# Performance work log

Hardware: AMD Instinct MI355X
Metric: run time of the kernel (lower is better)

The kernel has to match this reference:

```python
import math
import jax, jax.numpy as jnp
import numpy as np

B, S, D, E, K, H = 4, 1024, 768, 8, 2, 2048
NH_ROUTER, NH_COLLAB = 12, 2  # collab heads = min(n_heads, top_k) = 2
EPS = 1e-5


def setup_inputs() -> dict:
    key = jax.random.key(0)
    ks = jax.random.split(key, 16)
    n = lambda k, shp, s=0.02: jax.random.normal(k, shp, jnp.float32) * s
    return {
        "x": jax.random.normal(ks[0], (B, S, D), jnp.float32),
        # parallel expert params (E, D, H) / (E, H, D)
        "w1": n(ks[1], (E, D, H)), "w3": n(ks[2], (E, D, H)), "w2": n(ks[3], (E, H, D)),
        # router self-attention (torch MultiheadAttention packed qkv + out proj)
        "r_in_w": n(ks[4], (3 * D, D)), "r_in_b": jnp.zeros((3 * D,), jnp.float32),
        "r_out_w": n(ks[5], (D, D)), "r_out_b": jnp.zeros((D,), jnp.float32),
        "r_norm_w": jnp.ones((D,), jnp.float32),
        "gate_w": n(ks[6], (E, D)),
        # collaborative cross-attention
        "c_in_w": n(ks[7], (3 * D, D)), "c_in_b": jnp.zeros((3 * D,), jnp.float32),
        "c_out_w": n(ks[8], (D, D)), "c_out_b": jnp.zeros((D,), jnp.float32),
        "c_norm_w": jnp.ones((D,), jnp.float32),
        "ffn_w1": n(ks[9], (D, D)), "ffn_w2": n(ks[10], (D, D)),
        "o_w": n(ks[11], (D, D)),
    }


def _mha(x, in_w, in_b, out_w, out_b, nh):
    # torch nn.MultiheadAttention, batch_first, q=k=v=x; returns out and head-avg probs
    N, L, Dm = x.shape
    hd = Dm // nh
    qkv = x @ in_w.T + in_b                       # (N, L, 3D)
    q, k, v = jnp.split(qkv, 3, axis=-1)
    sp = lambda t: t.reshape(N, L, nh, hd).transpose(0, 2, 1, 3)
    q, k, v = sp(q), sp(k), sp(v)
    probs = jax.nn.softmax(jnp.einsum('nhld,nhmd->nhlm', q, k) / math.sqrt(hd), axis=-1)
    o = jnp.einsum('nhlm,nhmd->nhld', probs, v).transpose(0, 2, 1, 3).reshape(N, L, Dm)
    return o @ out_w.T + out_b, probs.mean(axis=1)


def _rms(x, w):
    return x * jax.lax.rsqrt(jnp.mean(x * x, axis=-1, keepdims=True) + EPS) * w


def reference(x, w1, w3, w2, r_in_w, r_in_b, r_out_w, r_out_b, r_norm_w, gate_w,
              c_in_w, c_in_b, c_out_w, c_out_b, c_norm_w, ffn_w1, ffn_w2, o_w):
    Bx, Sx, Dx = x.shape
    # dense all-expert SwiGLU: (B,S,E,D)
    gate = jnp.einsum('bsd,edh->bseh', x, w1)
    up = jnp.einsum('bsd,edh->bseh', x, w3)
    expert_out = jnp.einsum('bseh,ehd->bsed', jax.nn.silu(gate) * up, w2)
    ef = expert_out.reshape(Bx * Sx, E, Dx)
    # attention-based router over the E experts per token
    ctx, _ = _mha(ef, r_in_w, r_in_b, r_out_w, r_out_b, NH_ROUTER)
    ctx = _rms(ctx + ef, r_norm_w)
    logits = (ctx.mean(axis=1) @ gate_w.T).reshape(Bx, Sx, E)
    routing_probs = jax.nn.softmax(logits, axis=-1)
    tk_logits, tk_idx = jax.lax.top_k(logits, K)  # router_temperature = 1.0
    tk_probs = jax.nn.softmax(tk_logits, axis=-1)
    sel = jnp.take_along_axis(expert_out, tk_idx[..., None], axis=2)  # (B,S,K,D)
    sf = sel.reshape(Bx * Sx, K, Dx)
    # collaborative fusion among selected experts
    ao, aw = _mha(sf, c_in_w, c_in_b, c_out_w, c_out_b, NH_COLLAB)
    ao = _rms(ao + sf, c_norm_w)
    refined = (jax.nn.gelu(ao @ ffn_w1.T, approximate=False) @ ffn_w2.T) + ao
    refined = refined.reshape(Bx, Sx, K, Dx)
    final = jnp.sum(refined * tk_probs[..., None], axis=2) @ o_w.T
    # auxiliary loss
    usage = routing_probs.mean(axis=(0, 1))
    balance = jnp.mean((usage - usage.mean()) ** 2)
    diversity = jnp.mean(-jnp.sum(aw * jnp.log(aw + 1e-9), axis=-1))
    aux = 0.1 * (0.01 * diversity + 0.01 * balance)
    return final, aux, tk_idx
```

## Files before the change

### kernel.cpp

```cpp
#include <hip/hip_runtime.h>


typedef unsigned short u16;
typedef unsigned int u32;
typedef _Float16 f16;
typedef f16 f16x4 __attribute__((ext_vector_type(4)));
typedef f16 f16x8 __attribute__((ext_vector_type(8)));
typedef float f32x4 __attribute__((ext_vector_type(4)));

__device__ __forceinline__ float b2f(u16 v){
  union { u32 u; float f; } x; x.u = ((u32)v) << 16; return x.f;
}
__device__ __forceinline__ u16 f2b(float f){
  union { float f; u32 u; } x; x.f = f;
  u32 u = x.u;
  if ((u & 0x7fffffffu) > 0x7f800000u) return (u16)0x7fc0;
  return (u16)((u + 0x7fffu + ((u >> 16) & 1u)) >> 16);
}
__device__ __forceinline__ float gelu_f(float x){
  return 0.5f * x * (1.f + erff(x * 0.70710678118654752f));
}

template<int NW>
__device__ __forceinline__ float blockReduceSum(float v, float* red){
  #pragma unroll
  for (int o = 32; o > 0; o >>= 1) v += __shfl_down(v, o, 64);
  const int wv = threadIdx.x >> 6, ln = threadIdx.x & 63;
  __syncthreads();
  if (ln == 0) red[wv] = v;
  __syncthreads();
  float s = 0.f;
  #pragma unroll
  for (int i = 0; i < NW; i++) s += red[i];
  return s;
}

__device__ __forceinline__ float waveReduceSum(float v){
  #pragma unroll
  for (int o = 32; o > 0; o >>= 1) v += __shfl_xor(v, o, 64);
  return v;
}

template<int AK, bool SPLIT, bool BT, bool BIAS, int ACT, bool RES, bool DUAL, bool SK2>
__global__ __launch_bounds__(256, 2) void mgemm(
    const void* __restrict__ Ap, int lda, long long strideA,
    const float* __restrict__ B1, const float* __restrict__ B2, int ldb, long long strideB,
    float* __restrict__ C1, float* __restrict__ C2, int ldc, long long strideC,
    const float* __restrict__ bias, const float* __restrict__ resid, int ldr,
    int Kd, int zs)
{
  __shared__ f16 AsH[2][128*40];
  __shared__ f16 BsH[2][128*40];
  __shared__ f16 AsL[SPLIT ? 2 : 1][SPLIT ? 128*40 : 4];
  __shared__ f16 BsL[SPLIT ? 2 : 1][SPLIT ? 128*40 : 4];

  const int tid = threadIdx.x;
  const int m0 = blockIdx.y * 128, n0 = blockIdx.x * 128;
  const int z = blockIdx.z;
  int zi = z, k0 = 0, KL = Kd;
  const float* Bz; float* Cz;
  if constexpr (DUAL){
    if (z < zs){ zi = z;      Bz = B1 + (long long)zi*strideB; Cz = C1 + (long long)zi*strideC; }
    else       { zi = z - zs; Bz = B2 + (long long)zi*strideB; Cz = C2 + (long long)zi*strideC; }
  } else if constexpr (SK2){
    const int s = (z >= zs) ? 1 : 0;
    zi = z - s * zs;
    KL = Kd >> 1; k0 = s * KL;
    Bz = B1 + (long long)zi*strideB + (BT ? (long long)k0 : (long long)k0 * ldb);
    Cz = (s ? C2 : C1) + (long long)zi*strideC;
  } else {
    Bz = B1 + (long long)z*strideB; Cz = C1 + (long long)z*strideC;
  }
  const float* A32 = (const float*)Ap + (AK==0 ? (long long)zi*strideA : 0) + k0;
  const u16*   A16 = (const u16*)Ap   + (AK==1 ? (long long)zi*strideA : 0) + k0;

  const int ln = tid & 63, wv = tid >> 6;
  const int wm = (wv >> 1) * 64, wn = (wv & 1) * 64;
  const int fr = ln & 15, fq = ln >> 4;

  const int rA = tid >> 1, kcA = (tid & 1) * 16;
  const int npB = tid & 63, kgB = tid >> 6;

  f32x4 av[4]; uint4 av16[2]; f32x4 bv[4]; float2 bw[8];

  auto loadAB = [&](int kt){
    if constexpr (AK == 0){
      const float* s = A32 + (size_t)(m0 + rA) * lda + kt + kcA;
      av[0] = ((const f32x4*)s)[0]; av[1] = ((const f32x4*)s)[1];
      av[2] = ((const f32x4*)s)[2]; av[3] = ((const f32x4*)s)[3];
    } else {
      const u16* s = A16 + (size_t)(m0 + rA) * lda + kt + kcA;
      av16[0] = ((const uint4*)s)[0]; av16[1] = ((const uint4*)s)[1];
    }
    if constexpr (BT){
      const float* s = Bz + (size_t)(n0 + rA) * ldb + kt + kcA;
      bv[0] = ((const f32x4*)s)[0]; bv[1] = ((const f32x4*)s)[1];
      bv[2] = ((const f32x4*)s)[2]; bv[3] = ((const f32x4*)s)[3];
    } else {
      const float* s = Bz + (size_t)(kt + kgB * 8) * ldb + n0 + 2 * npB;
      #pragma unroll
      for (int kk = 0; kk < 8; kk++) bw[kk] = *(const float2*)(s + (size_t)kk * ldb);
    }
  };

  auto storeAB = [&](int b){
    if constexpr (AK == 0){
      #pragma unroll
      for (int jj = 0; jj < 2; jj++){
        f16x8 h, l;
        #pragma unroll
        for (int c = 0; c < 8; c++){
          const float v = av[jj*2 + (c>>2)][c & 3];
          h[c] = (f16)v;
          if constexpr (SPLIT) l[c] = (f16)(v - (float)h[c]);
        }
        *(f16x8*)&AsH[b][rA*40 + kcA + jj*8] = h;
        if constexpr (SPLIT) *(f16x8*)&AsL[b][rA*40 + kcA + jj*8] = l;
      }
    } else {
      #pragma unroll
      for (int j = 0; j < 2; j++){
        const uint4 v = av16[j];
        f16x8 h;
        h[0]=(f16)b2f((u16)(v.x & 0xffff)); h[1]=(f16)b2f((u16)(v.x >> 16));
        h[2]=(f16)b2f((u16)(v.y & 0xffff)); h[3]=(f16)b2f((u16)(v.y >> 16));
        h[4]=(f16)b2f((u16)(v.z & 0xffff)); h[5]=(f16)b2f((u16)(v.z >> 16));
        h[6]=(f16)b2f((u16)(v.w & 0xffff)); h[7]=(f16)b2f((u16)(v.w >> 16));
        *(f16x8*)&AsH[b][rA*40 + kcA + j*8] = h;
      }
    }
    if constexpr (BT){
      #pragma unroll
      for (int jj = 0; jj < 2; jj++){
        f16x8 h, l;
        #pragma unroll
        for (int c = 0; c < 8; c++){
          const float v = bv[jj*2 + (c>>2)][c & 3];
          h[c] = (f16)v;
          if constexpr (SPLIT) l[c] = (f16)(v - (float)h[c]);
        }
        *(f16x8*)&BsH[b][rA*40 + kcA + jj*8] = h;
        if constexpr (SPLIT) *(f16x8*)&BsL[b][rA*40 + kcA + jj*8] = l;
      }
    } else {
      #pragma unroll
      for (int c = 0; c < 2; c++){
        const int row = 2*npB + c;
        const int p8 = (kgB + (row >> 2)) & 3;
        f16x8 h, l;
        #pragma unroll
        for (int kk = 0; kk < 8; kk++){
          const float v = c ? bw[kk].y : bw[kk].x;
          h[kk] = (f16)v;
          if constexpr (SPLIT) l[kk] = (f16)(v - (float)h[kk]);
        }
        *(f16x8*)&BsH[b][row*40 + p8*8] = h;
        if constexpr (SPLIT) *(f16x8*)&BsL[b][row*40 + p8*8] = l;
      }
    }
  };

  f32x4 acc[4][4];
  #pragma unroll
  for (int i = 0; i < 4; i++)
    #pragma unroll
    for (int j = 0; j < 4; j++){ acc[i][j][0]=0.f; acc[i][j][1]=0.f; acc[i][j][2]=0.f; acc[i][j][3]=0.f; }

  int aoff[4], boff[4];
  #pragma unroll
  for (int i = 0; i < 4; i++) aoff[i] = (wm + i*16 + fr)*40 + fq*8;
  #pragma unroll
  for (int j = 0; j < 4; j++){
    const int brow = wn + j*16 + fr;
    boff[j] = brow*40 + (BT ? fq*8 : (((fq + (brow >> 2)) & 3) << 3));
  }

  loadAB(0);
  const int NT = KL >> 5;
  for (int t = 0; t < NT; t++){
    const int b = t & 1;
    storeAB(b);
    __syncthreads();
    if (t + 1 < NT) loadAB((t + 1) << 5);
    f16x8 aH[4], bH[4];
    #pragma unroll
    for (int i = 0; i < 4; i++) aH[i] = *(const f16x8*)&AsH[b][aoff[i]];
    #pragma unroll
    for (int j = 0; j < 4; j++) bH[j] = *(const f16x8*)&BsH[b][boff[j]];
    #pragma unroll
    for (int i = 0; i < 4; i++)
      #pragma unroll
      for (int j = 0; j < 4; j++)
        acc[i][j] = __builtin_amdgcn_mfma_f32_16x16x32_f16(aH[i], bH[j], acc[i][j], 0, 0, 0);
    if constexpr (SPLIT){
      f16x8 aL[4], bL[4];
      #pragma unroll
      for (int i = 0; i < 4; i++) aL[i] = *(const f16x8*)&AsL[b][aoff[i]];
      #pragma unroll
      for (int j = 0; j < 4; j++) bL[j] = *(const f16x8*)&BsL[b][boff[j]];
      #pragma unroll
      for (int i = 0; i < 4; i++)
        #pragma unroll
        for (int j = 0; j < 4; j++){
          acc[i][j] = __builtin_amdgcn_mfma_f32_16x16x32_f16(aH[i], bL[j], acc[i][j], 0, 0, 0);
          acc[i][j] = __builtin_amdgcn_mfma_f32_16x16x32_f16(aL[i], bH[j], acc[i][j], 0, 0, 0);
        }
    }
  }

  #pragma unroll
  for (int j = 0; j < 4; j++){
    const int n = n0 + wn + j*16 + fr;
    float bvv = 0.f;
    if constexpr (BIAS) bvv = bias[n];
    #pragma unroll
    for (int i = 0; i < 4; i++){
      #pragma unroll
      for (int r = 0; r < 4; r++){
        const int m = m0 + wm + i*16 + fq*4 + r;
        float v = acc[i][j][r];
        if constexpr (BIAS) v += bvv;
        if constexpr (ACT == 1) v = gelu_f(v);
        if constexpr (RES) v += resid[(size_t)m * ldr + n];
        Cz[(size_t)m * ldc + n] = v;
      }
    }
  }
}

__global__ void silu_k(const float4* __restrict__ g, const float4* __restrict__ u,
                       float4* __restrict__ h, int n4){
  const int i = blockIdx.x * 256 + threadIdx.x;
  if (i < n4){
    const float4 gv = g[i], uv = u[i];
    float4 r;
    r.x = (gv.x / (1.f + expf(-gv.x))) * uv.x;
    r.y = (gv.y / (1.f + expf(-gv.y))) * uv.y;
    r.z = (gv.z / (1.f + expf(-gv.z))) * uv.z;
    r.w = (gv.w / (1.f + expf(-gv.w))) * uv.w;
    h[i] = r;
  }
}

template<int ACT, bool RES, bool BIAS>
__global__ void add2_k(float* __restrict__ dst, const float* __restrict__ src,
                       const float* __restrict__ bias, const float* __restrict__ resid,
                       int n4, int ld4){
  const int i = blockIdx.x * 256 + threadIdx.x;
  if (i >= n4) return;
  const f32x4 a = ((const f32x4*)dst)[i];
  const f32x4 b = ((const f32x4*)src)[i];
  const int c4 = (i % ld4) * 4;
  f32x4 r;
  #pragma unroll
  for (int c = 0; c < 4; c++){
    float v = a[c] + b[c];
    if constexpr (BIAS) v += bias[c4 + c];
    if constexpr (ACT == 1) v = gelu_f(v);
    if constexpr (RES) v += resid[(size_t)i * 4 + c];
    r[c] = v;
  }
  ((f32x4*)dst)[i] = r;
}

__global__ __launch_bounds__(128) void router_attn(const float* __restrict__ qkv,
                                                   float* __restrict__ attn_o){
  __shared__ float L[8 * 1536];
  __shared__ float Ps[96][8];
  const int t = blockIdx.x, tid = threadIdx.x;
  const float* src = qkv + (size_t)t * 8 * 2304;
  for (int i = tid; i < 3072; i += 128){
    const int e = i / 384, c4 = i - e * 384;
    ((float4*)L)[i] = ((const float4*)(src + (size_t)e * 2304))[c4];
  }
  __syncthreads();
  if (tid < 96){
    const int h = tid >> 3, e = tid & 7;
    const float* q = L + e * 1536 + h * 64;
    float s[8]; float mx = -1e30f;
    #pragma unroll
    for (int e2 = 0; e2 < 8; e2++){
      const float* kk = L + e2 * 1536 + 768 + h * 64;
      float acc = 0.f;
      #pragma unroll
      for (int d = 0; d < 64; d++) acc = fmaf(q[d], kk[d], acc);
      s[e2] = acc * 0.125f;
      mx = fmaxf(mx, s[e2]);
    }
    float den = 0.f;
    #pragma unroll
    for (int e2 = 0; e2 < 8; e2++){ s[e2] = expf(s[e2] - mx); den += s[e2]; }
    const float inv = 1.f / den;
    #pragma unroll
    for (int e2 = 0; e2 < 8; e2++) Ps[tid][e2] = s[e2] * inv;
  }
  __syncthreads();
  for (int i = tid; i < 1536; i += 128){
    const int e = i / 192, c4 = i - e * 192;
    ((float4*)L)[i] = ((const float4*)(src + (size_t)e * 2304 + 1536))[c4];
  }
  __syncthreads();
  if (tid < 96){
    const int h = tid >> 3, e = tid & 7;
    float p[8];
    #pragma unroll
    for (int e2 = 0; e2 < 8; e2++) p[e2] = Ps[tid][e2];
    float* dst = attn_o + ((size_t)t * 8 + e) * 768 + h * 64;
    for (int d = 0; d < 64; d++){
      float acc = 0.f;
      #pragma unroll
      for (int e2 = 0; e2 < 8; e2++) acc = fmaf(p[e2], L[e2 * 768 + h * 64 + d], acc);
      dst[d] = acc;
    }
  }
}

__global__ __launch_bounds__(256) void router_final(
    const float* __restrict__ proj, const float* __restrict__ eoc,
    const float* __restrict__ rnw, const float* __restrict__ gw,
    int t0, float* __restrict__ usage, float* __restrict__ tkp,
    u16* __restrict__ sf, float* __restrict__ oidx)
{
  const int wv = threadIdx.x >> 6, ln = threadIdx.x & 63;
  const int tl = blockIdx.x * 4 + wv, t = t0 + tl;

  float rw[12];
  #pragma unroll
  for (int g = 0; g < 3; g++){
    const f32x4 w = ((const f32x4*)rnw)[ln + g * 64];
    #pragma unroll
    for (int c = 0; c < 4; c++) rw[g*4 + c] = w[c];
  }

  float cs[12];
  #pragma unroll
  for (int i = 0; i < 12; i++) cs[i] = 0.f;

  for (int e = 0; e < 8; e++){
    const float* pr = proj + ((size_t)tl * 8 + e) * 768;
    const float* er = eoc  + ((size_t)tl * 8 + e) * 768;
    float v[12]; float ss = 0.f;
    #pragma unroll
    for (int g = 0; g < 3; g++){
      const f32x4 a = ((const f32x4*)pr)[ln + g * 64];
      const f32x4 b = ((const f32x4*)er)[ln + g * 64];
      #pragma unroll
      for (int c = 0; c < 4; c++){ const float vv = a[c] + b[c]; v[g*4 + c] = vv; ss += vv * vv; }
    }
    ss = waveReduceSum(ss);
    const float sc = 1.f / sqrtf(ss * (1.f / 768.f) + 1e-5f);
    #pragma unroll
    for (int i = 0; i < 12; i++) cs[i] += v[i] * sc * rw[i];
  }

  float lg[8];
  #pragma unroll
  for (int j = 0; j < 8; j++){
    const float* gwr = gw + j * 768;
    float p = 0.f;
    #pragma unroll
    for (int g = 0; g < 3; g++){
      const f32x4 w = ((const f32x4*)gwr)[ln + g * 64];
      #pragma unroll
      for (int c = 0; c < 4; c++) p += cs[g*4 + c] * w[c];
    }
    lg[j] = waveReduceSum(p) * 0.125f;
  }

  int i0 = 0; float l0 = lg[0];
  #pragma unroll
  for (int j = 1; j < 8; j++) if (lg[j] > l0){ l0 = lg[j]; i0 = j; }
  int i1 = -1; float l1 = -1e30f;
  #pragma unroll
  for (int j = 0; j < 8; j++) if (j != i0 && lg[j] > l1){ l1 = lg[j]; i1 = j; }

  if (ln == 0){
    float mx = -1e30f;
    #pragma unroll
    for (int j = 0; j < 8; j++) mx = fmaxf(mx, lg[j]);
    float ex[8], den = 0.f;
    #pragma unroll
    for (int j = 0; j < 8; j++){ ex[j] = expf(lg[j] - mx); den += ex[j]; }
    const float inv = 1.f / den;
    #pragma unroll
    for (int j = 0; j < 8; j++) atomicAdd(&usage[j], ex[j] * inv);
    const float e1 = expf(l1 - l0);
    const float p0 = 1.f / (1.f + e1);
    tkp[(size_t)t * 2]     = p0;
    tkp[(size_t)t * 2 + 1] = e1 * p0;
    oidx[(size_t)t * 2]     = (float)i0;
    oidx[(size_t)t * 2 + 1] = (float)i1;
  }

  #pragma unroll
  for (int s = 0; s < 2; s++){
    const int ie = s ? i1 : i0;
    const float* er = eoc + ((size_t)tl * 8 + ie) * 768;
    #pragma unroll
    for (int g = 0; g < 3; g++){
      const f32x4 a = ((const f32x4*)er)[ln + g * 64];
      ushort4 o;
      o.x = f2b(a[0]); o.y = f2b(a[1]); o.z = f2b(a[2]); o.w = f2b(a[3]);
      *(ushort4*)&sf[((size_t)t * 2 + s) * 768 + 4 * (ln + g * 64)] = o;
    }
  }
}

__global__ __launch_bounds__(128) void collab_attn(
    const float* __restrict__ qkv, float* __restrict__ attn_o, float* __restrict__ divsum)
{
  const int t = blockIdx.x, tid = threadIdx.x;
  __shared__ float L[4608];
  __shared__ float P[8];
  __shared__ float red[2];
  const float* src = qkv + (size_t)t * 4608;
  for (int i = tid; i < 4608; i += 128) L[i] = src[i];
  __syncthreads();
  for (int hij = 0; hij < 8; hij++){
    const int h = hij >> 2, qi = (hij >> 1) & 1, kj = hij & 1;
    const float* q = L + qi * 2304 + h * 384;
    const float* k = L + kj * 2304 + 768 + h * 384;
    float acc = 0.f;
    for (int d = tid; d < 384; d += 128) acc += q[d] * k[d];
    acc = blockReduceSum<2>(acc, red);
    if (tid == 0) P[hij] = acc;
  }
  __syncthreads();
  if (tid == 0){
    const float scale = 0.051031036307982884f;
    float aw[2][2] = {{0.f,0.f},{0.f,0.f}};
    for (int h = 0; h < 2; h++)
      for (int i = 0; i < 2; i++){
        const float s0 = P[h*4 + i*2 + 0] * scale, s1 = P[h*4 + i*2 + 1] * scale;
        const float m = fmaxf(s0, s1);
        const float e0 = expf(s0 - m), e1 = expf(s1 - m), inv = 1.f / (e0 + e1);
        P[h*4 + i*2 + 0] = e0 * inv; P[h*4 + i*2 + 1] = e1 * inv;
        aw[i][0] += 0.5f * e0 * inv; aw[i][1] += 0.5f * e1 * inv;
      }
    float ent = 0.f;
    for (int i = 0; i < 2; i++)
      for (int j = 0; j < 2; j++) ent -= aw[i][j] * logf(aw[i][j] + 1e-9f);
    atomicAdd(divsum, ent);
  }
  __syncthreads();
  for (int c = tid; c < 768; c += 128){
    const int h = c / 384;
    const float v0 = L[1536 + c], v1 = L[3840 + c];
    attn_o[((size_t)t * 2 + 0) * 768 + c] = P[h*4 + 0] * v0 + P[h*4 + 1] * v1;
    attn_o[((size_t)t * 2 + 1) * 768 + c] = P[h*4 + 2] * v0 + P[h*4 + 3] * v1;
  }
}

__global__ __launch_bounds__(256) void rms_k(const float* __restrict__ a, const u16* __restrict__ b,
                                             const float* __restrict__ wt, float* __restrict__ o){
  const int r = blockIdx.x, tid = threadIdx.x;
  __shared__ float red[4];
  float v[3]; float ss = 0.f;
  #pragma unroll
  for (int i = 0; i < 3; i++){
    const int c = tid + i * 256;
    v[i] = a[(size_t)r * 768 + c] + b2f(b[(size_t)r * 768 + c]);
    ss += v[i] * v[i];
  }
  ss = blockReduceSum<4>(ss, red);
  const float sc = 1.f / sqrtf(ss * (1.f / 768.f) + 1e-5f);
  #pragma unroll
  for (int i = 0; i < 3; i++){
    const int c = tid + i * 256;
    o[(size_t)r * 768 + c] = v[i] * sc * wt[c];
  }
}

__global__ void wsum(const float* __restrict__ refined, const float* __restrict__ tkp,
                     float* __restrict__ y){
  const int idx = blockIdx.x * 256 + threadIdx.x;
  const int t = idx / 768, c = idx - t * 768;
  const float r0 = refined[((size_t)t * 2) * 768 + c];
  const float r1 = refined[((size_t)t * 2 + 1) * 768 + c];
  y[idx] = tkp[t * 2] * r0 + tkp[t * 2 + 1] * r1;
}

__global__ void aux_k(const float* __restrict__ usage, const float* __restrict__ divsum,
                      float* __restrict__ out){
  if (threadIdx.x == 0 && blockIdx.x == 0){
    float u[8], s = 0.f;
    for (int e = 0; e < 8; e++){ u[e] = usage[e] * (1.f / 4096.f); s += u[e]; }
    const float mean = s * 0.125f;
    float bal = 0.f;
    for (int e = 0; e < 8; e++){ const float d = u[e] - mean; bal += d * d; }
    bal *= 0.125f;
    const float div = divsum[0] * (1.f / 8192.f);
    out[0] = 0.1f * (0.01f * div + 0.01f * bal);
  }
}

__global__ void zero_k(float* p, int n){
  const int i = blockIdx.x * 64 + threadIdx.x;
  if (i < n) p[i] = 0.f;
}

extern "C" void kernel_launch(void* const* d_in, const int* in_sizes, int n_in,
                              void* d_out, int out_size, void* d_ws, size_t ws_size,
                              hipStream_t stream)
{
  (void)in_sizes; (void)n_in; (void)out_size; (void)ws_size;
  const float* x       = (const float*)d_in[0];
  const float* w1      = (const float*)d_in[1];
  const float* w3      = (const float*)d_in[2];
  const float* w2      = (const float*)d_in[3];
  const float* r_in_w  = (const float*)d_in[4];
  const float* r_in_b  = (const float*)d_in[5];
  const float* r_out_w = (const float*)d_in[6];
  const float* r_out_b = (const float*)d_in[7];
  const float* r_norm_w= (const float*)d_in[8];
  const float* gate_w  = (const float*)d_in[9];
  const float* c_in_w  = (const float*)d_in[10];
  const float* c_in_b  = (const float*)d_in[11];
  const float* c_out_w = (const float*)d_in[12];
  const float* c_out_b = (const float*)d_in[13];
  const float* c_norm_w= (const float*)d_in[14];
  const float* ffn_w1  = (const float*)d_in[15];
  const float* ffn_w2  = (const float*)d_in[16];
  const float* o_w     = (const float*)d_in[17];

  char* wsb   = (char*)d_ws;
  char* arena = wsb;
  float* eoc  = (float*)(wsb + 33554432);
  u16*   sf   = (u16*)  (wsb + 39845888);
  float* tkp  = (float*)(wsb + 52428800);
  float* usage= (float*)(wsb + 52461568);

  float* gateb = (float*)(arena);
  float* upb   = (float*)(arena + 16777216);
  float* qkvr  = (float*)(arena);
  float* aor   = (float*)(arena + 18874368);
  float* projr = (float*)(arena + 25165824);

  float* qkvc  = (float*)(arena);
  float* aoc   = (float*)(arena + 18874368);
  float* projc = (float*)(arena + 25165824);
  float* aob   = (float*)(arena);
  float* t1b   = (float*)(arena + 6291456);
  float* refb  = (float*)(arena + 12582912);
  float* ybuf  = (float*)(arena + 18874368);

  float* outp    = (float*)d_out;
  float* out_aux = outp + (size_t)4096*768;
  float* out_idx = out_aux + 1;

  zero_k<<<1, 64, 0, stream>>>(usage, 16);

  for (int cch = 0; cch < 16; cch++){
    const int t0 = cch * 256;
    mgemm<0,true,false,false,0,false,true,false><<<dim3(16,2,16),256,0,stream>>>(
      x + (size_t)t0*768, 768, 0LL,
      w1, w3, 2048, 1572864LL,
      gateb, upb, 2048, 524288LL,
      nullptr, nullptr, 0, 768, 8);
    silu_k<<<4096, 256, 0, stream>>>((const float4*)gateb, (const float4*)upb,
                                     (float4*)gateb, 1048576);
    mgemm<0,true,false,false,0,false,false,true><<<dim3(6,2,16),256,0,stream>>>(
      gateb, 2048, 524288LL,
      w2, nullptr, 768, 1572864LL,
      eoc, upb, 6144, 768LL,
      nullptr, nullptr, 0, 2048, 8);
    add2_k<0,false,false><<<1536, 256, 0, stream>>>(eoc, upb, nullptr, nullptr, 393216, 192);
    mgemm<0,true,true,true,0,false,false,false><<<dim3(18,16,1),256,0,stream>>>(
      eoc, 768, 0LL, r_in_w, nullptr, 768, 0LL,
      qkvr, nullptr, 2304, 0LL, r_in_b, nullptr, 0, 768, 0);
    router_attn<<<256, 128, 0, stream>>>(qkvr, aor);
    mgemm<0,true,true,false,0,false,false,true><<<dim3(6,16,2),256,0,stream>>>(
      aor, 768, 0LL, r_out_w, nullptr, 768, 0LL,
      projr, qkvr, 768, 0LL, nullptr, nullptr, 0, 768, 1);
    add2_k<0,false,true><<<1536, 256, 0, stream>>>(projr, qkvr, r_out_b, nullptr, 393216, 192);
    router_final<<<64, 256, 0, stream>>>(projr, eoc, r_norm_w, gate_w, t0,
                                         usage, tkp, sf, out_idx);
  }

  for (int q = 0; q < 4; q++){
    const int tq0 = q * 1024;
    const u16* sf_q = sf + (size_t)tq0 * 2 * 768;
    mgemm<1,false,true,true,0,false,false,false><<<dim3(18,16,1),256,0,stream>>>(
      sf_q, 768, 0LL, c_in_w, nullptr, 768, 0LL,
      qkvc, nullptr, 2304, 0LL, c_in_b, nullptr, 0, 768, 0);
    collab_attn<<<1024, 128, 0, stream>>>(qkvc, aoc, usage + 8);
    mgemm<0,false,true,false,0,false,false,true><<<dim3(6,16,2),256,0,stream>>>(
      aoc, 768, 0LL, c_out_w, nullptr, 768, 0LL,
      projc, qkvc, 768, 0LL, nullptr, nullptr, 0, 768, 1);
    add2_k<0,false,true><<<1536, 256, 0, stream>>>(projc, qkvc, c_out_b, nullptr, 393216, 192);
    rms_k<<<2048, 256, 0, stream>>>(projc, sf_q, c_norm_w, aob);
    mgemm<0,false,true,false,0,false,false,true><<<dim3(6,16,2),256,0,stream>>>(
      aob, 768, 0LL, ffn_w1, nullptr, 768, 0LL,
      t1b, refb, 768, 0LL, nullptr, nullptr, 0, 768, 1);
    add2_k<1,false,false><<<1536, 256, 0, stream>>>(t1b, refb, nullptr, nullptr, 393216, 192);
    mgemm<0,false,true,false,0,false,false,true><<<dim3(6,16,2),256,0,stream>>>(
      t1b, 768, 0LL, ffn_w2, nullptr, 768, 0LL,
      refb, projc, 768, 0LL, nullptr, nullptr, 0, 768, 1);
    add2_k<0,true,false><<<1536, 256, 0, stream>>>(refb, projc, nullptr, aob, 393216, 192);
    wsum<<<3072, 256, 0, stream>>>(refb, tkp + (size_t)tq0 * 2, ybuf);
    mgemm<0,false,true,false,0,false,false,true><<<dim3(6,8,2),256,0,stream>>>(
      ybuf, 768, 0LL, o_w, nullptr, 768, 0LL,
      outp + (size_t)tq0 * 768, t1b, 768, 0LL, nullptr, nullptr, 0, 768, 1);
    add2_k<0,false,false><<<768, 256, 0, stream>>>(outp + (size_t)tq0 * 768, t1b, nullptr, nullptr, 196608, 192);
  }
  aux_k<<<1, 64, 0, stream>>>(usage, usage + 8, out_aux);
}
```

Measured before the change: 4.209 ms.

## Fuse split-K reductions and elementwise ops into GEMM A-loads and consumers

Adds an A-operand prologue to the GEMM that combines two fp32 inputs while loading (SiLU*up, add of split-K partials, add+GELU). This removes the standalone silu and add2 passes, and downstream kernels (router_final, rms2, wsum3) now consume both split-K partials plus the bias directly. The main loop is restructured into a two-register-set double-buffered pipeline, and the LDS swizzle for the non-transposed B operand is changed. The cost is extra registers and redundant reads of the partial buffers in the consumers, and the output buffer is reused as scratch for the w2 partial.

```diff
diff --git a/kernel.cpp b/kernel.cpp
--- a/kernel.cpp
+++ b/kernel.cpp
@@ -41,9 +41,9 @@
   return v;
 }
 
-template<int AK, bool SPLIT, bool BT, bool BIAS, int ACT, bool RES, bool DUAL, bool SK2>
+template<int AK, int AOP, bool SPLIT, bool BT, bool BIAS, int ACT, bool RES, bool DUAL, bool SK2>
 __global__ __launch_bounds__(256, 2) void mgemm(
-    const void* __restrict__ Ap, int lda, long long strideA,
+    const void* __restrict__ Ap, const float* __restrict__ A2p, int lda, long long strideA,
     const float* __restrict__ B1, const float* __restrict__ B2, int ldb, long long strideB,
     float* __restrict__ C1, float* __restrict__ C2, int ldc, long long strideC,
     const float* __restrict__ bias, const float* __restrict__ resid, int ldr,
@@ -71,8 +71,9 @@
   } else {
     Bz = B1 + (long long)z*strideB; Cz = C1 + (long long)z*strideC;
   }
-  const float* A32 = (const float*)Ap + (AK==0 ? (long long)zi*strideA : 0) + k0;
-  const u16*   A16 = (const u16*)Ap   + (AK==1 ? (long long)zi*strideA : 0) + k0;
+  const float* A32  = (const float*)Ap + (AK==0 ? (long long)zi*strideA : 0) + k0;
+  const u16*   A16  = (const u16*)Ap   + (AK==1 ? (long long)zi*strideA : 0) + k0;
+  const float* A32b = (AOP != 0) ? (A2p + (long long)zi*strideA + k0) : nullptr;
 
   const int ln = tid & 63, wv = tid >> 6;
   const int wm = (wv >> 1) * 64, wn = (wv & 1) * 64;
@@ -81,36 +82,52 @@
   const int rA = tid >> 1, kcA = (tid & 1) * 16;
   const int npB = tid & 63, kgB = tid >> 6;
 
-  f32x4 av[4]; uint4 av16[2]; f32x4 bv[4]; float2 bw[8];
-
-  auto loadAB = [&](int kt){
+  struct Regs {
+    f32x4 av[4]; f32x4 av2[4]; uint4 av16[2]; f32x4 bv[4]; float2 bw[8];
+  };
+  Regs R0, R1;
+
+  auto loadAB = [&](Regs& R, int kt){
     if constexpr (AK == 0){
       const float* s = A32 + (size_t)(m0 + rA) * lda + kt + kcA;
-      av[0] = ((const f32x4*)s)[0]; av[1] = ((const f32x4*)s)[1];
-      av[2] = ((const f32x4*)s)[2]; av[3] = ((const f32x4*)s)[3];
+      #pragma unroll
+      for (int j = 0; j < 4; j++) R.av[j] = ((const f32x4*)s)[j];
+      if constexpr (AOP != 0){
+        const float* s2 = A32b + (size_t)(m0 + rA) * lda + kt + kcA;
+        #pragma unroll
+        for (int j = 0; j < 4; j++) R.av2[j] = ((const f32x4*)s2)[j];
+      }
     } else {
       const u16* s = A16 + (size_t)(m0 + rA) * lda + kt + kcA;
-      av16[0] = ((const uint4*)s)[0]; av16[1] = ((const uint4*)s)[1];
+      R.av16[0] = ((const uint4*)s)[0]; R.av16[1] = ((const uint4*)s)[1];
     }
     if constexpr (BT){
       const float* s = Bz + (size_t)(n0 + rA) * ldb + kt + kcA;
-      bv[0] = ((const f32x4*)s)[0]; bv[1] = ((const f32x4*)s)[1];
-      bv[2] = ((const f32x4*)s)[2]; bv[3] = ((const f32x4*)s)[3];
+      #pragma unroll
+      for (int j = 0; j < 4; j++) R.bv[j] = ((const f32x4*)s)[j];
     } else {
       const float* s = Bz + (size_t)(kt + kgB * 8) * ldb + n0 + 2 * npB;
       #pragma unroll
-      for (int kk = 0; kk < 8; kk++) bw[kk] = *(const float2*)(s + (size_t)kk * ldb);
+      for (int kk = 0; kk < 8; kk++) R.bw[kk] = *(const float2*)(s + (size_t)kk * ldb);
     }
   };
 
-  auto storeAB = [&](int b){
+  auto storeAB = [&](const Regs& R, int b){
     if constexpr (AK == 0){
       #pragma unroll
       for (int jj = 0; jj < 2; jj++){
         f16x8 h, l;
         #pragma unroll
         for (int c = 0; c < 8; c++){
-          const float v = av[jj*2 + (c>>2)][c & 3];
+          float v = R.av[jj*2 + (c>>2)][c & 3];
+          if constexpr (AOP == 1){
+            const float u = R.av2[jj*2 + (c>>2)][c & 3];
+            v = (v / (1.f + expf(-v))) * u;
+          } else if constexpr (AOP == 2){
+            v = v + R.av2[jj*2 + (c>>2)][c & 3];
+          } else if constexpr (AOP == 3){
+            v = gelu_f(v + R.av2[jj*2 + (c>>2)][c & 3]);
+          }
           h[c] = (f16)v;
           if constexpr (SPLIT) l[c] = (f16)(v - (float)h[c]);
         }
@@ -120,7 +137,7 @@
     } else {
       #pragma unroll
       for (int j = 0; j < 2; j++){
-        const uint4 v = av16[j];
+        const uint4 v = R.av16[j];
         f16x8 h;
         h[0]=(f16)b2f((u16)(v.x & 0xffff)); h[1]=(f16)b2f((u16)(v.x >> 16));
         h[2]=(f16)b2f((u16)(v.y & 0xffff)); h[3]=(f16)b2f((u16)(v.y >> 16));
@@ -135,7 +152,7 @@
         f16x8 h, l;
         #pragma unroll
         for (int c = 0; c < 8; c++){
-          const float v = bv[jj*2 + (c>>2)][c & 3];
+          const float v = R.bv[jj*2 + (c>>2)][c & 3];
           h[c] = (f16)v;
           if constexpr (SPLIT) l[c] = (f16)(v - (float)h[c]);
         }
@@ -146,11 +163,11 @@
       #pragma unroll
       for (int c = 0; c < 2; c++){
         const int row = 2*npB + c;
-        const int p8 = (kgB + (row >> 2)) & 3;
+        const int p8 = (kgB + (row >> 3)) & 3;
         f16x8 h, l;
         #pragma unroll
         for (int kk = 0; kk < 8; kk++){
-          const float v = c ? bw[kk].y : bw[kk].x;
+          const float v = c ? R.bw[kk].y : R.bw[kk].x;
           h[kk] = (f16)v;
           if constexpr (SPLIT) l[kk] = (f16)(v - (float)h[kk]);
         }
@@ -172,16 +189,10 @@
   #pragma unroll
   for (int j = 0; j < 4; j++){
     const int brow = wn + j*16 + fr;
-    boff[j] = brow*40 + (BT ? fq*8 : (((fq + (brow >> 2)) & 3) << 3));
-  }
-
-  loadAB(0);
-  const int NT = KL >> 5;
-  for (int t = 0; t < NT; t++){
-    const int b = t & 1;
-    storeAB(b);
-    __syncthreads();
-    if (t + 1 < NT) loadAB((t + 1) << 5);
+    boff[j] = brow*40 + (BT ? fq*8 : (((fq + (brow >> 3)) & 3) << 3));
+  }
+
+  auto compute = [&](int b){
     f16x8 aH[4], bH[4];
     #pragma unroll
     for (int i = 0; i < 4; i++) aH[i] = *(const f16x8*)&AsH[b][aoff[i]];
@@ -206,6 +217,20 @@
           acc[i][j] = __builtin_amdgcn_mfma_f32_16x16x32_f16(aL[i], bH[j], acc[i][j], 0, 0, 0);
         }
     }
+  };
+
+  const int NT = KL >> 5;
+  loadAB(R0, 0);
+  loadAB(R1, 32);
+  for (int tt = 0; tt < NT; tt += 2){
+    storeAB(R0, 0);
+    __syncthreads();
+    if (tt + 2 < NT) loadAB(R0, (tt + 2) << 5);
+    compute(0);
+    storeAB(R1, 1);
+    __syncthreads();
+    if (tt + 3 < NT) loadAB(R1, (tt + 3) << 5);
+    compute(1);
   }
 
   #pragma unroll
@@ -225,20 +250,6 @@
         Cz[(size_t)m * ldc + n] = v;
       }
     }
-  }
-}
-
-__global__ void silu_k(const float4* __restrict__ g, const float4* __restrict__ u,
-                       float4* __restrict__ h, int n4){
-  const int i = blockIdx.x * 256 + threadIdx.x;
-  if (i < n4){
-    const float4 gv = g[i], uv = u[i];
-    float4 r;
-    r.x = (gv.x / (1.f + expf(-gv.x))) * uv.x;
-    r.y = (gv.y / (1.f + expf(-gv.y))) * uv.y;
-    r.z = (gv.z / (1.f + expf(-gv.z))) * uv.z;
-    r.w = (gv.w / (1.f + expf(-gv.w))) * uv.w;
-    h[i] = r;
   }
 }
 
@@ -265,7 +276,7 @@
 
 __global__ __launch_bounds__(128) void router_attn(const float* __restrict__ qkv,
                                                    float* __restrict__ attn_o){
-  __shared__ float L[8 * 1536];
+  __shared__ __align__(16) float L[8 * 1536];
   __shared__ float Ps[96][8];
   const int t = blockIdx.x, tid = threadIdx.x;
   const float* src = qkv + (size_t)t * 8 * 2304;
@@ -316,7 +327,9 @@
 }
 
 __global__ __launch_bounds__(256) void router_final(
-    const float* __restrict__ proj, const float* __restrict__ eoc,
+    const float* __restrict__ proj0, const float* __restrict__ proj1,
+    const float* __restrict__ pbias,
+    const float* __restrict__ eoc0, const float* __restrict__ eoc1,
     const float* __restrict__ rnw, const float* __restrict__ gw,
     int t0, float* __restrict__ usage, float* __restrict__ tkp,
     u16* __restrict__ sf, float* __restrict__ oidx)
@@ -324,12 +337,13 @@
   const int wv = threadIdx.x >> 6, ln = threadIdx.x & 63;
   const int tl = blockIdx.x * 4 + wv, t = t0 + tl;
 
-  float rw[12];
+  float rw[12], pb[12];
   #pragma unroll
   for (int g = 0; g < 3; g++){
     const f32x4 w = ((const f32x4*)rnw)[ln + g * 64];
-    #pragma unroll
-    for (int c = 0; c < 4; c++) rw[g*4 + c] = w[c];
+    const f32x4 bbv = ((const f32x4*)pbias)[ln + g * 64];
+    #pragma unroll
+    for (int c = 0; c < 4; c++){ rw[g*4 + c] = w[c]; pb[g*4 + c] = bbv[c]; }
   }
 
   float cs[12];
@@ -337,15 +351,19 @@
   for (int i = 0; i < 12; i++) cs[i] = 0.f;
 
   for (int e = 0; e < 8; e++){
-    const float* pr = proj + ((size_t)tl * 8 + e) * 768;
-    const float* er = eoc  + ((size_t)tl * 8 + e) * 768;
+    const size_t ro = ((size_t)tl * 8 + e) * 768;
     float v[12]; float ss = 0.f;
     #pragma unroll
     for (int g = 0; g < 3; g++){
-      const f32x4 a = ((const f32x4*)pr)[ln + g * 64];
-      const f32x4 b = ((const f32x4*)er)[ln + g * 64];
-      #pragma unroll
-      for (int c = 0; c < 4; c++){ const float vv = a[c] + b[c]; v[g*4 + c] = vv; ss += vv * vv; }
+      const f32x4 p0 = ((const f32x4*)(proj0 + ro))[ln + g * 64];
+      const f32x4 p1 = ((const f32x4*)(proj1 + ro))[ln + g * 64];
+      const f32x4 e0 = ((const f32x4*)(eoc0 + ro))[ln + g * 64];
+      const f32x4 e1 = ((const f32x4*)(eoc1 + ro))[ln + g * 64];
+      #pragma unroll
+      for (int c = 0; c < 4; c++){
+        const float vv = ((p0[c] + p1[c]) + pb[g*4 + c]) + (e0[c] + e1[c]);
+        v[g*4 + c] = vv; ss += vv * vv;
+      }
     }
     ss = waveReduceSum(ss);
     const float sc = 1.f / sqrtf(ss * (1.f / 768.f) + 1e-5f);
@@ -384,10 +402,10 @@
     const float inv = 1.f / den;
     #pragma unroll
     for (int j = 0; j < 8; j++) atomicAdd(&usage[j], ex[j] * inv);
-    const float e1 = expf(l1 - l0);
-    const float p0 = 1.f / (1.f + e1);
+    const float e1v = expf(l1 - l0);
+    const float p0 = 1.f / (1.f + e1v);
     tkp[(size_t)t * 2]     = p0;
-    tkp[(size_t)t * 2 + 1] = e1 * p0;
+    tkp[(size_t)t * 2 + 1] = e1v * p0;
     oidx[(size_t)t * 2]     = (float)i0;
     oidx[(size_t)t * 2 + 1] = (float)i1;
   }
@@ -395,12 +413,14 @@
   #pragma unroll
   for (int s = 0; s < 2; s++){
     const int ie = s ? i1 : i0;
-    const float* er = eoc + ((size_t)tl * 8 + ie) * 768;
+    const size_t ro = ((size_t)tl * 8 + ie) * 768;
     #pragma unroll
     for (int g = 0; g < 3; g++){
-      const f32x4 a = ((const f32x4*)er)[ln + g * 64];
+      const f32x4 a = ((const f32x4*)(eoc0 + ro))[ln + g * 64];
+      const f32x4 b = ((const f32x4*)(eoc1 + ro))[ln + g * 64];
       ushort4 o;
-      o.x = f2b(a[0]); o.y = f2b(a[1]); o.z = f2b(a[2]); o.w = f2b(a[3]);
+      o.x = f2b(a[0] + b[0]); o.y = f2b(a[1] + b[1]);
+      o.z = f2b(a[2] + b[2]); o.w = f2b(a[3] + b[3]);
       *(ushort4*)&sf[((size_t)t * 2 + s) * 768 + 4 * (ln + g * 64)] = o;
     }
   }
@@ -410,11 +430,11 @@
     const float* __restrict__ qkv, float* __restrict__ attn_o, float* __restrict__ divsum)
 {
   const int t = blockIdx.x, tid = threadIdx.x;
-  __shared__ float L[4608];
+  __shared__ __align__(16) float L[4608];
   __shared__ float P[8];
   __shared__ float red[2];
   const float* src = qkv + (size_t)t * 4608;
-  for (int i = tid; i < 4608; i += 128) L[i] = src[i];
+  for (int i = tid; i < 1152; i += 128) ((float4*)L)[i] = ((const float4*)src)[i];
   __syncthreads();
   for (int hij = 0; hij < 8; hij++){
     const int h = hij >> 2, qi = (hij >> 1) & 1, kj = hij & 1;
@@ -451,15 +471,18 @@
   }
 }
 
-__global__ __launch_bounds__(256) void rms_k(const float* __restrict__ a, const u16* __restrict__ b,
-                                             const float* __restrict__ wt, float* __restrict__ o){
+__global__ __launch_bounds__(256) void rms2_k(
+    const float* __restrict__ a0, const float* __restrict__ a1,
+    const float* __restrict__ bb, const u16* __restrict__ rb,
+    const float* __restrict__ wt, float* __restrict__ o){
   const int r = blockIdx.x, tid = threadIdx.x;
   __shared__ float red[4];
   float v[3]; float ss = 0.f;
   #pragma unroll
   for (int i = 0; i < 3; i++){
     const int c = tid + i * 256;
-    v[i] = a[(size_t)r * 768 + c] + b2f(b[(size_t)r * 768 + c]);
+    const float t = (a0[(size_t)r * 768 + c] + a1[(size_t)r * 768 + c]) + bb[c];
+    v[i] = t + b2f(rb[(size_t)r * 768 + c]);
     ss += v[i] * v[i];
   }
   ss = blockReduceSum<4>(ss, red);
@@ -471,13 +494,15 @@
   }
 }
 
-__global__ void wsum(const float* __restrict__ refined, const float* __restrict__ tkp,
-                     float* __restrict__ y){
+__global__ void wsum3(const float* __restrict__ pA, const float* __restrict__ pB,
+                      const float* __restrict__ ao, const float* __restrict__ tkp,
+                      float* __restrict__ y){
   const int idx = blockIdx.x * 256 + threadIdx.x;
   const int t = idx / 768, c = idx - t * 768;
-  const float r0 = refined[((size_t)t * 2) * 768 + c];
-  const float r1 = refined[((size_t)t * 2 + 1) * 768 + c];
-  y[idx] = tkp[t * 2] * r0 + tkp[t * 2 + 1] * r1;
+  const size_t r0 = ((size_t)t * 2) * 768 + c, r1 = r0 + 768;
+  const float v0 = (pA[r0] + pB[r0]) + ao[r0];
+  const float v1 = (pA[r1] + pB[r1]) + ao[r1];
+  y[idx] = tkp[t * 2] * v0 + tkp[t * 2 + 1] * v1;
 }
 
 __global__ void aux_k(const float* __restrict__ usage, const float* __restrict__ divsum,
@@ -535,73 +560,71 @@
   float* qkvr  = (float*)(arena);
   float* aor   = (float*)(arena + 18874368);
   float* projr = (float*)(arena + 25165824);
+  float* pr2   = (float*)(arena);
 
   float* qkvc  = (float*)(arena);
   float* aoc   = (float*)(arena + 18874368);
-  float* projc = (float*)(arena + 25165824);
-  float* aob   = (float*)(arena);
-  float* t1b   = (float*)(arena + 6291456);
-  float* refb  = (float*)(arena + 12582912);
-  float* ybuf  = (float*)(arena + 18874368);
+  float* pc1   = (float*)(arena + 25165824);
+  float* pc2   = (float*)(arena);
+  float* aob   = (float*)(arena + 6291456);
+  float* pf1   = (float*)(arena + 12582912);
+  float* pf2   = (float*)(arena + 18874368);
+  float* ybuf  = (float*)(arena + 12582912);
+  float* fo2   = (float*)(arena + 18874368);
 
   float* outp    = (float*)d_out;
   float* out_aux = outp + (size_t)4096*768;
   float* out_idx = out_aux + 1;
+  float* w2p2    = outp;
 
   zero_k<<<1, 64, 0, stream>>>(usage, 16);
 
   for (int cch = 0; cch < 16; cch++){
     const int t0 = cch * 256;
-    mgemm<0,true,false,false,0,false,true,false><<<dim3(16,2,16),256,0,stream>>>(
-      x + (size_t)t0*768, 768, 0LL,
+    mgemm<0,0,true,false,false,0,false,true,false><<<dim3(16,2,16),256,0,stream>>>(
+      x + (size_t)t0*768, nullptr, 768, 0LL,
       w1, w3, 2048, 1572864LL,
       gateb, upb, 2048, 524288LL,
       nullptr, nullptr, 0, 768, 8);
-    silu_k<<<4096, 256, 0, stream>>>((const float4*)gateb, (const float4*)upb,
-                                     (float4*)gateb, 1048576);
-    mgemm<0,true,false,false,0,false,false,true><<<dim3(6,2,16),256,0,stream>>>(
-      gateb, 2048, 524288LL,
+    mgemm<0,1,true,false,false,0,false,false,true><<<dim3(6,2,16),256,0,stream>>>(
+      gateb, upb, 2048, 524288LL,
       w2, nullptr, 768, 1572864LL,
-      eoc, upb, 6144, 768LL,
+      eoc, w2p2, 6144, 768LL,
       nullptr, nullptr, 0, 2048, 8);
-    add2_k<0,false,false><<<1536, 256, 0, stream>>>(eoc, upb, nullptr, nullptr, 393216, 192);
-    mgemm<0,true,true,true,0,false,false,false><<<dim3(18,16,1),256,0,stream>>>(
-      eoc, 768, 0LL, r_in_w, nullptr, 768, 0LL,
+    mgemm<0,2,true,true,true,0,false,false,false><<<dim3(18,16,1),256,0,stream>>>(
+      eoc, w2p2, 768, 0LL, r_in_w, nullptr, 768, 0LL,
       qkvr, nullptr, 2304, 0LL, r_in_b, nullptr, 0, 768, 0);
     router_attn<<<256, 128, 0, stream>>>(qkvr, aor);
-    mgemm<0,true,true,false,0,false,false,true><<<dim3(6,16,2),256,0,stream>>>(
-      aor, 768, 0LL, r_out_w, nullptr, 768, 0LL,
-      projr, qkvr, 768, 0LL, nullptr, nullptr, 0, 768, 1);
-    add2_k<0,false,true><<<1536, 256, 0, stream>>>(projr, qkvr, r_out_b, nullptr, 393216, 192);
-    router_final<<<64, 256, 0, stream>>>(projr, eoc, r_norm_w, gate_w, t0,
-                                         usage, tkp, sf, out_idx);
+    mgemm<0,0,true,true,false,0,false,false,true><<<dim3(6,16,2),256,0,stream>>>(
+      aor, nullptr, 768, 0LL, r_out_w, nullptr, 768, 0LL,
+      projr, pr2, 768, 0LL, nullptr, nullptr, 0, 768, 1);
+    router_final<<<64, 256, 0, stream>>>(projr, pr2, r_out_b, eoc, w2p2,
+                                         r_norm_w, gate_w, t0, usage, tkp, sf, out_idx);
   }
 
   for (int q = 0; q < 4; q++){
     const int tq0 = q * 1024;
     const u16* sf_q = sf + (size_t)tq0 * 2 * 768;
-    mgemm<1,false,true,true,0,false,false,false><<<dim3(18,16,1),256,0,stream>>>(
-      sf_q, 768, 0LL, c_in_w, nullptr, 768, 0LL,
+    mgemm<1,0,false,true,true,0,false,false,false><<<dim3(18,16,1),256,0,stream>>>(
+      sf_q, nullptr, 768, 0LL, c_in_w, nullptr, 768, 0LL,
       qkvc, nullptr, 2304, 0LL, c_in_b, nullptr, 0, 768, 0);
     collab_attn<<<1024, 128, 0, stream>>>(qkvc, aoc, usage + 8);
-    mgemm<0,false,true,false,0,false,false,true><<<dim3(6,16,2),256,0,stream>>>(
-      aoc, 768, 0LL, c_out_w, nullptr, 768, 0LL,
-      projc, qkvc, 768, 0LL, nullptr, nullptr, 0, 768, 1);
-    add2_k<0,false,true><<<1536, 256, 0, stream>>>(projc, qkvc, c_out_b, nullptr, 393216, 192);
-    rms_k<<<2048, 256, 0, stream>>>(projc, sf_q, c_norm_w, aob);
-    mgemm<0,false,true,false,0,false,false,true><<<dim3(6,16,2),256,0,stream>>>(
-      aob, 768, 0LL, ffn_w1, nullptr, 768, 0LL,
-      t1b, refb, 768, 0LL, nullptr, nullptr, 0, 768, 1);
-    add2_k<1,false,false><<<1536, 256, 0, stream>>>(t1b, refb, nullptr, nullptr, 393216, 192);
-    mgemm<0,false,true,false,0,false,false,true><<<dim3(6,16,2),256,0,stream>>>(
-      t1b, 768, 0LL, ffn_w2, nullptr, 768, 0LL,
-      refb, projc, 768, 0LL, nullptr, nullptr, 0, 768, 1);
-    add2_k<0,true,false><<<1536, 256, 0, stream>>>(refb, projc, nullptr, aob, 393216, 192);
-    wsum<<<3072, 256, 0, stream>>>(refb, tkp + (size_t)tq0 * 2, ybuf);
-    mgemm<0,false,true,false,0,false,false,true><<<dim3(6,8,2),256,0,stream>>>(
-      ybuf, 768, 0LL, o_w, nullptr, 768, 0LL,
-      outp + (size_t)tq0 * 768, t1b, 768, 0LL, nullptr, nullptr, 0, 768, 1);
-    add2_k<0,false,false><<<768, 256, 0, stream>>>(outp + (size_t)tq0 * 768, t1b, nullptr, nullptr, 196608, 192);
+    mgemm<0,0,false,true,false,0,false,false,true><<<dim3(6,16,2),256,0,stream>>>(
+      aoc, nullptr, 768, 0LL, c_out_w, nullptr, 768, 0LL,
+      pc1, pc2, 768, 0LL, nullptr, nullptr, 0, 768, 1);
+    rms2_k<<<2048, 256, 0, stream>>>(pc1, pc2, c_out_b, sf_q, c_norm_w, aob);
+    mgemm<0,0,false,true,false,0,false,false,true><<<dim3(6,16,2),256,0,stream>>>(
+      aob, nullptr, 768, 0LL, ffn_w1, nullptr, 768, 0LL,
+      pf1, pf2, 768, 0LL, nullptr, nullptr, 0, 768, 1);
+    mgemm<0,3,false,true,false,0,false,false,true><<<dim3(6,16,2),256,0,stream>>>(
+      pf1, pf2, 768, 0LL, ffn_w2, nullptr, 768, 0LL,
+      pc1, pc2, 768, 0LL, nullptr, nullptr, 0, 768, 1);
+    wsum3<<<3072, 256, 0, stream>>>(pc1, pc2, aob, tkp + (size_t)tq0 * 2, ybuf);
+    mgemm<0,0,false,true,false,0,false,false,true><<<dim3(6,8,2),256,0,stream>>>(
+      ybuf, nullptr, 768, 0LL, o_w, nullptr, 768, 0LL,
+      outp + (size_t)tq0 * 768, fo2, 768, 0LL, nullptr, nullptr, 0, 768, 1);
+    add2_k<0,false,false><<<768, 256, 0, stream>>>(outp + (size_t)tq0 * 768, fo2,
+                                                   nullptr, nullptr, 196608, 192);
   }
   aux_k<<<1, 64, 0, stream>>>(usage, usage + 8, out_aux);
 }
```

Result: slower. 5.980 ms (+42.1%).
